# Optimization experiments

Hardware: AMD Instinct MI355X
Metric: run time of the kernel (lower is better)

The kernel has to match this reference:

```python
import jax, jax.numpy as jnp
import numpy as np

N_NODES = 100000
N_EDGES = 1600000
D_IN, D_H, D_OUT = 512, 128, 64
BN_EPS = 1e-5


def setup_inputs() -> dict:
    key = jax.random.key(0)
    ks = jax.random.split(key, 8)
    x = jax.random.normal(ks[0], (N_NODES, D_IN), dtype=jnp.float32)
    # COO sparse normalized adjacency
    row = jnp.sort(jax.random.randint(ks[1], (N_EDGES,), 0, N_NODES))
    col = jax.random.randint(ks[2], (N_EDGES,), 0, N_NODES)
    adj_vals = jax.random.uniform(ks[3], (N_EDGES,), dtype=jnp.float32) / 16.0
    # GraphConvolution params (xavier_uniform weight, zero bias)
    lim0 = float(np.sqrt(6.0 / (D_IN + D_H)))
    lim1 = float(np.sqrt(6.0 / (D_H + D_OUT)))
    W0 = jax.random.uniform(ks[4], (D_IN, D_H), minval=-lim0, maxval=lim0, dtype=jnp.float32)
    W1 = jax.random.uniform(ks[5], (D_H, D_OUT), minval=-lim1, maxval=lim1, dtype=jnp.float32)
    b0 = jnp.zeros((D_H,), dtype=jnp.float32)
    b1 = jnp.zeros((D_OUT,), dtype=jnp.float32)
    return {"x": x, "W0": W0, "b0": b0, "W1": W1, "b1": b1,
            "adj_vals": adj_vals, "row": row, "col": col}


def _spmm(vals, row, col, h, n):
    # (sparse adj) @ h : gather source rows, scale by edge value, scatter-add to dest
    return jax.ops.segment_sum(vals[:, None] * h[col], row, num_segments=n)


def reference(x, W0, b0, W1, b1, adj_vals, row, col):
    n = x.shape[0]
    # layer 0: adj @ (x @ W0) + b0  (dropout is identity in eval mode)
    h = _spmm(adj_vals, row, col, x @ W0, n) + b0
    h = jax.nn.relu(h)
    # BatchNorm1d(affine=False, track_running_stats=False): batch stats, biased var
    mean = jnp.mean(h, axis=0)
    var = jnp.mean(jnp.square(h - mean), axis=0)
    h = (h - mean) * jax.lax.rsqrt(var + BN_EPS)
    # layer 1: adj @ (h @ W1) + b1
    return _spmm(adj_vals, row, col, h @ W1, n) + b1
```

## Files before the change

kernel.cpp:

```cpp
#include <hip/hip_runtime.h>
#include <hip/hip_bf16.h>
#include <cstdint>
#include <cstddef>

#define D_IN  512
#define D_H   128
#define D_OUT 64
#define SB    512

typedef __attribute__((ext_vector_type(8))) short bf16x8;
typedef __attribute__((ext_vector_type(4))) float f32x4;

__device__ __forceinline__ float bf2f(unsigned short u) {
  union { unsigned int i; float f; } v; v.i = ((unsigned int)u) << 16; return v.f;
}
__device__ __forceinline__ unsigned short f2bf(float f) {
  union { unsigned int i; float f; } v; v.f = f;
  unsigned int r = v.i + 0x7FFFu + ((v.i >> 16) & 1u);
  return (unsigned short)(r >> 16);
}
__device__ __forceinline__ unsigned int pk_bf16(float a, float b) {
  union { __hip_bfloat162 h; unsigned int u; } cv;
  cv.h = __float22bfloat162_rn(make_float2(a, b));
  return cv.u;
}

#define OFF_RP    0u
#define OFF_W0T   400384u
#define OFF_W1TP  531456u
#define OFF_CVEC  547840u
#define OFF_PSUM  548096u
#define OFF_PSQ   810240u
#define OFF_H     1072384u
#define END_H     26672384u
#define END_HW    39472384u

__global__ void k_init(const int* __restrict__ row, int* __restrict__ rp,
                       const float* __restrict__ W0, unsigned short* __restrict__ W0t,
                       int n, int e, int RB) {
  int b = blockIdx.x, t = threadIdx.x;
  if (b < RB) {
    int i = b * 256 + t;
    if (i > n) return;
    int lo = 0, hi = e;
    while (lo < hi) { int mid = (lo + hi) >> 1; if (row[mid] < i) lo = mid + 1; else hi = mid; }
    rp[i] = lo;
  } else {
    int idx = (b - RB) * 256 + t;
    int k = idx & (D_IN - 1);
    int nn = idx >> 9;
    W0t[nn * D_IN + k] = f2bf(W0[k * D_H + nn]);
  }
}

__global__ __launch_bounds__(256) void k_gemm1(const float* __restrict__ A,
                                               const unsigned short* __restrict__ Bt,
                                               unsigned short* __restrict__ C,
                                               int M) {
  __shared__ unsigned short Ash[2][4 * 128 * 8];
  __shared__ unsigned short Bsh[2][4 * 128 * 8];
  const int tid  = threadIdx.x;
  const int lane = tid & 63;
  const int wave = tid >> 6;
  const int wm = (wave >> 1) * 64;
  const int wn = (wave & 1) * 64;
  const int m0 = blockIdx.x * 128;
  const int quad = lane >> 4;
  const int l16  = lane & 15;
  f32x4 acc[4][4] = {};

  int am[2], ak[2];
  const float* aptr[2];
  const unsigned short* bptr[2];
#pragma unroll
  for (int i = 0; i < 2; ++i) {
    int c = tid + i * 256;
    am[i] = c >> 2; ak[i] = c & 3;
    int gm = m0 + am[i]; if (gm >= M) gm = M - 1;
    aptr[i] = A  + (size_t)gm * D_IN + ak[i] * 8;
    bptr[i] = Bt + (size_t)am[i] * D_IN + ak[i] * 8;
  }

  f32x4 areg[2][2];
  bf16x8 breg[2];
#pragma unroll
  for (int i = 0; i < 2; ++i) {
    areg[i][0] = *(const f32x4*)(aptr[i]);
    areg[i][1] = *(const f32x4*)(aptr[i] + 4);
    breg[i]    = *(const bf16x8*)(bptr[i]);
  }

  const int NIT = D_IN / 32;
  for (int it = 0; it < NIT; ++it) {
    const int buf = it & 1;
    unsigned short* ash = Ash[buf];
    unsigned short* bsh = Bsh[buf];
#pragma unroll
    for (int i = 0; i < 2; ++i) {
      unsigned int pk4[4];
      pk4[0] = pk_bf16(areg[i][0][0], areg[i][0][1]);
      pk4[1] = pk_bf16(areg[i][0][2], areg[i][0][3]);
      pk4[2] = pk_bf16(areg[i][1][0], areg[i][1][1]);
      pk4[3] = pk_bf16(areg[i][1][2], areg[i][1][3]);
      *(uint4*)&ash[(ak[i] * 128 + am[i]) * 8] = *(uint4*)pk4;
      *(bf16x8*)&bsh[(ak[i] * 128 + am[i]) * 8] = breg[i];
    }
    __syncthreads();
    if (it + 1 < NIT) {
      int k0 = (it + 1) * 32;
#pragma unroll
      for (int i = 0; i < 2; ++i) {
        areg[i][0] = *(const f32x4*)(aptr[i] + k0);
        areg[i][1] = *(const f32x4*)(aptr[i] + k0 + 4);
        breg[i]    = *(const bf16x8*)(bptr[i] + k0);
      }
    }
    bf16x8 af[4], bfv[4];
#pragma unroll
    for (int mf = 0; mf < 4; ++mf)
      af[mf] = *(const bf16x8*)&ash[(quad * 128 + (wm + mf * 16 + l16)) * 8];
#pragma unroll
    for (int nf = 0; nf < 4; ++nf)
      bfv[nf] = *(const bf16x8*)&bsh[(quad * 128 + (wn + nf * 16 + l16)) * 8];
#pragma unroll
    for (int mf = 0; mf < 4; ++mf)
#pragma unroll
      for (int nf = 0; nf < 4; ++nf)
        acc[mf][nf] = __builtin_amdgcn_mfma_f32_16x16x32_bf16(af[mf], bfv[nf], acc[mf][nf], 0, 0, 0);
  }
#pragma unroll
  for (int mf = 0; mf < 4; ++mf)
#pragma unroll
    for (int nf = 0; nf < 4; ++nf)
#pragma unroll
      for (int i = 0; i < 4; ++i) {
        int r = m0 + wm + mf * 16 + quad * 4 + i;
        int cc = wn + nf * 16 + l16;
        if (r < M) C[(size_t)r * D_H + cc] = f2bf(acc[mf][nf][i]);
      }
}

__global__ __launch_bounds__(256) void k_spmm1(const unsigned int* __restrict__ xw2,
                                               const float* __restrict__ adj,
                                               const int* __restrict__ col,
                                               const int* __restrict__ rp,
                                               const float* __restrict__ b0,
                                               unsigned int* __restrict__ h2,
                                               int n) {
  int node = blockIdx.x * 4 + (threadIdx.x >> 6);
  if (node >= n) return;
  int l = threadIdx.x & 63;
  int e0 = rp[node], e1 = rp[node + 1];
  float a0 = 0.f, a1 = 0.f;
  for (int e = e0; e < e1; e += 16) {
    int idx[16]; float w[16];
#pragma unroll
    for (int j = 0; j < 16; ++j) {
      int ee = e + j;
      int ec = ee < e1 ? ee : e0;
      idx[j] = col[ec];
      w[j] = ee < e1 ? adj[ec] : 0.f;
    }
#pragma unroll
    for (int j = 0; j < 16; ++j) {
      unsigned int p = xw2[(size_t)idx[j] * 64 + l];
      a0 += w[j] * bf2f((unsigned short)(p & 0xFFFF));
      a1 += w[j] * bf2f((unsigned short)(p >> 16));
    }
  }
  float r0 = fmaxf(a0 + b0[2 * l], 0.f);
  float r1 = fmaxf(a1 + b0[2 * l + 1], 0.f);
  h2[(size_t)node * 64 + l] = ((unsigned int)f2bf(r1) << 16) | (unsigned int)f2bf(r0);
}

__global__ __launch_bounds__(256) void k_stats(const unsigned int* __restrict__ h2,
                                               float* __restrict__ psum,
                                               float* __restrict__ psq, int n) {
  __shared__ float sA[256], sB[256], qA[256], qB[256];
  int t = threadIdx.x;
  int f2 = t & 63, rg = t >> 6;
  float s0 = 0.f, s1 = 0.f, q0 = 0.f, q1 = 0.f;
  for (int r = blockIdx.x * 4 + rg; r < n; r += gridDim.x * 4) {
    unsigned int p = h2[(size_t)r * 64 + f2];
    float v0 = bf2f((unsigned short)(p & 0xFFFF));
    float v1 = bf2f((unsigned short)(p >> 16));
    s0 += v0; s1 += v1; q0 += v0 * v0; q1 += v1 * v1;
  }
  sA[t] = s0; sB[t] = s1; qA[t] = q0; qB[t] = q1;
  __syncthreads();
  if (t < 64) {
    float S0 = sA[t] + sA[t + 64] + sA[t + 128] + sA[t + 192];
    float S1 = sB[t] + sB[t + 64] + sB[t + 128] + sB[t + 192];
    float Q0 = qA[t] + qA[t + 64] + qA[t + 128] + qA[t + 192];
    float Q1 = qB[t] + qB[t + 64] + qB[t + 128] + qB[t + 192];
    psum[blockIdx.x * 128 + 2 * t]     = S0;
    psum[blockIdx.x * 128 + 2 * t + 1] = S1;
    psq [blockIdx.x * 128 + 2 * t]     = Q0;
    psq [blockIdx.x * 128 + 2 * t + 1] = Q1;
  }
}

__global__ void k_prep2(const float* __restrict__ psum, const float* __restrict__ psq,
                        const float* __restrict__ W1,
                        unsigned short* __restrict__ W1tp, float* __restrict__ cvec,
                        int n) {
  __shared__ float mean_s[128], istd_s[128];
  int t = threadIdx.x;
  if (t < 128) {
    float s = 0.f, q = 0.f;
#pragma unroll 4
    for (int b = 0; b < SB; ++b) { s += psum[b * 128 + t]; q += psq[b * 128 + t]; }
    float m = s / (float)n;
    float var = q / (float)n - m * m;
    if (var < 0.f) var = 0.f;
    mean_s[t] = m;
    istd_s[t] = rsqrtf(var + 1e-5f);
  }
  __syncthreads();
  for (int idx = t; idx < D_OUT * D_H; idx += 256) {
    int nn = idx >> 7, k = idx & 127;
    W1tp[nn * D_H + k] = f2bf(istd_s[k] * W1[k * D_OUT + nn]);
  }
  if (t < D_OUT) {
    float a = 0.f;
    for (int k = 0; k < D_H; ++k) a += mean_s[k] * istd_s[k] * W1[k * D_OUT + t];
    cvec[t] = -a;
  }
}

__global__ __launch_bounds__(256) void k_gemm2(const unsigned short* __restrict__ A,
                                               const unsigned short* __restrict__ Bt,
                                               const float* __restrict__ cvec,
                                               unsigned short* __restrict__ Cout,
                                               int M) {
  __shared__ unsigned short Ash[4 * 128 * 8];
  __shared__ unsigned short Bsh[4 * 64 * 8];
  const int tid  = threadIdx.x;
  const int lane = tid & 63;
  const int wave = tid >> 6;
  const int wm = wave * 32;
  const int m0 = blockIdx.x * 128;
  const int quad = lane >> 4;
  const int l16  = lane & 15;
  f32x4 acc[2][4] = {};

  for (int k0 = 0; k0 < D_H; k0 += 32) {
    __syncthreads();
#pragma unroll
    for (int i = 0; i < 2; ++i) {
      int c = tid + i * 256;
      int m = c >> 2, k8 = c & 3;
      int gm = m0 + m; if (gm >= M) gm = M - 1;
      *(bf16x8*)&Ash[(k8 * 128 + m) * 8] =
          *(const bf16x8*)&A[(size_t)gm * D_H + k0 + k8 * 8];
    }
    {
      int nn = tid >> 2, k8 = tid & 3;
      *(bf16x8*)&Bsh[(k8 * 64 + nn) * 8] =
          *(const bf16x8*)&Bt[(size_t)nn * D_H + k0 + k8 * 8];
    }
    __syncthreads();
    bf16x8 af[2], bfv[4];
#pragma unroll
    for (int mf = 0; mf < 2; ++mf)
      af[mf] = *(const bf16x8*)&Ash[(quad * 128 + (wm + mf * 16 + l16)) * 8];
#pragma unroll
    for (int nf = 0; nf < 4; ++nf)
      bfv[nf] = *(const bf16x8*)&Bsh[(quad * 64 + (nf * 16 + l16)) * 8];
#pragma unroll
    for (int mf = 0; mf < 2; ++mf)
#pragma unroll
      for (int nf = 0; nf < 4; ++nf)
        acc[mf][nf] = __builtin_amdgcn_mfma_f32_16x16x32_bf16(af[mf], bfv[nf], acc[mf][nf], 0, 0, 0);
  }
#pragma unroll
  for (int mf = 0; mf < 2; ++mf)
#pragma unroll
    for (int nf = 0; nf < 4; ++nf)
#pragma unroll
      for (int i = 0; i < 4; ++i) {
        int r = m0 + wm + mf * 16 + quad * 4 + i;
        int cc = nf * 16 + l16;
        if (r < M) Cout[(size_t)r * 64 + cc] = f2bf(acc[mf][nf][i] + cvec[cc]);
      }
}

__global__ __launch_bounds__(256) void k_spmm2(const unsigned int* __restrict__ hw2,
                                               const float* __restrict__ adj,
                                               const int* __restrict__ col,
                                               const int* __restrict__ rp,
                                               const float* __restrict__ b1,
                                               float2* __restrict__ o2,
                                               int n) {
  int node = blockIdx.x * 8 + (threadIdx.x >> 5);
  if (node >= n) return;
  int l = threadIdx.x & 31;
  int e0 = rp[node], e1 = rp[node + 1];
  float a0 = 0.f, a1 = 0.f;
  for (int e = e0; e < e1; e += 16) {
    int idx[16]; float w[16];
#pragma unroll
    for (int j = 0; j < 16; ++j) {
      int ee = e + j;
      int ec = ee < e1 ? ee : e0;
      idx[j] = col[ec];
      w[j] = ee < e1 ? adj[ec] : 0.f;
    }
#pragma unroll
    for (int j = 0; j < 16; ++j) {
      unsigned int p = hw2[(size_t)idx[j] * 32 + l];
      a0 += w[j] * bf2f((unsigned short)(p & 0xFFFF));
      a1 += w[j] * bf2f((unsigned short)(p >> 16));
    }
  }
  float2 r; r.x = a0 + b1[2 * l]; r.y = a1 + b1[2 * l + 1];
  o2[(size_t)node * 32 + l] = r;
}

extern "C" void kernel_launch(void* const* d_in, const int* in_sizes, int n_in,
                              void* d_out, int out_size, void* d_ws, size_t ws_size,
                              hipStream_t stream) {
  const float* x   = (const float*)d_in[0];
  const float* W0  = (const float*)d_in[1];
  const float* b0  = (const float*)d_in[2];
  const float* W1  = (const float*)d_in[3];
  const float* b1  = (const float*)d_in[4];
  const float* adj = (const float*)d_in[5];
  const int* row = (const int*)d_in[6];
  const int* col = (const int*)d_in[7];
  const int N = in_sizes[0] / D_IN;
  const int E = in_sizes[5];

  char* ws = (char*)d_ws;
  int*            rp   = (int*)(ws + OFF_RP);
  unsigned short* W0t  = (unsigned short*)(ws + OFF_W0T);
  unsigned short* W1tp = (unsigned short*)(ws + OFF_W1TP);
  float*          cvec = (float*)(ws + OFF_CVEC);
  float*          psum = (float*)(ws + OFF_PSUM);
  float*          psq  = (float*)(ws + OFF_PSQ);
  unsigned short* h    = (unsigned short*)(ws + OFF_H);

  unsigned short* xw = (unsigned short*)d_out;
  const bool hw_in_ws = (ws_size >= (size_t)END_HW);
  unsigned short* hw   = hw_in_ws ? (unsigned short*)(ws + END_H) : (unsigned short*)d_out;
  float*          outd = hw_in_ws ? (float*)d_out                 : (float*)(ws + OFF_H);

  const int RB = (N + 1 + 255) / 256;
  const int TB = (D_IN * D_H) / 256;
  k_init<<<RB + TB, 256, 0, stream>>>(row, rp, W0, W0t, N, E, RB);

  k_gemm1<<<(N + 127) / 128, 256, 0, stream>>>(x, W0t, xw, N);
  k_spmm1<<<(N + 3) / 4, 256, 0, stream>>>((const unsigned int*)xw, adj, col, rp, b0,
                                           (unsigned int*)h, N);
  k_stats<<<SB, 256, 0, stream>>>((const unsigned int*)h, psum, psq, N);
  k_prep2<<<1, 256, 0, stream>>>(psum, psq, W1, W1tp, cvec, N);
  k_gemm2<<<(N + 127) / 128, 256, 0, stream>>>(h, W1tp, cvec, hw, N);
  k_spmm2<<<(N + 7) / 8, 256, 0, stream>>>((const unsigned int*)hw, adj, col, rp, b1,
                                           (float2*)outd, N);

  if (!hw_in_ws) {
    hipMemcpyAsync(d_out, outd, (size_t)N * D_OUT * sizeof(float),
                   hipMemcpyDeviceToDevice, stream);
  }
}
```

Before: 515.5 us.

## Fuse GCN pipeline into one cooperative persistent kernel with grid syncs

Replaces the seven-kernel launch sequence with a single cooperative kernel of 512 persistent blocks. Each phase (row pointers, GEMM1, SpMM1 with fused BN statistics, BN prep, GEMM2, SpMM2) loops over tiles and is separated by grid-wide syncs. This removes per-kernel launch overhead and the separate stats pass over h, since stats are accumulated during SpMM1. The cost is a fixed grid size that may limit occupancy and latency hiding in the gather-heavy SpMM phases, plus grid.sync overhead, with the old path kept as a fallback.

```diff
diff --git a/kernel.cpp b/kernel.cpp
--- a/kernel.cpp
+++ b/kernel.cpp
@@ -1,11 +1,15 @@
 #include <hip/hip_runtime.h>
+#include <hip/hip_cooperative_groups.h>
 #include <hip/hip_bf16.h>
 #include <cstdint>
 #include <cstddef>
 
+namespace cg = cooperative_groups;
+
 #define D_IN  512
 #define D_H   128
 #define D_OUT 64
+#define GRID  512
 #define SB    512
 
 typedef __attribute__((ext_vector_type(8))) short bf16x8;
@@ -34,6 +38,275 @@
 #define OFF_H     1072384u
 #define END_H     26672384u
 #define END_HW    39472384u
+
+__global__ __launch_bounds__(256, 2) void gcn_mega(
+    const float* __restrict__ x, const float* __restrict__ W0,
+    const float* __restrict__ b0, const float* __restrict__ W1,
+    const float* __restrict__ b1, const float* __restrict__ adj,
+    const int* __restrict__ row, const int* __restrict__ col,
+    char* __restrict__ ws, unsigned short* __restrict__ xw16,
+    float2* __restrict__ outv, int N, int E) {
+  __shared__ union {
+    struct { unsigned short A[2][4096]; unsigned short B[2][4096]; } g1;
+    struct { float sA[256], sB[256], qA[256], qB[256]; } st;
+    struct { unsigned short A[4096]; unsigned short B[2048]; } g2;
+    struct { float mean[128]; float istd[128]; } pp;
+  } sh;
+
+  cg::grid_group grid = cg::this_grid();
+  const int G   = gridDim.x;
+  const int bid = blockIdx.x;
+  const int tid = threadIdx.x;
+  const int lane = tid & 63;
+  const int wave = tid >> 6;
+  const int quad = lane >> 4;
+  const int l16  = lane & 15;
+
+  int*            rp   = (int*)(ws + OFF_RP);
+  unsigned short* W0t  = (unsigned short*)(ws + OFF_W0T);
+  unsigned short* W1tp = (unsigned short*)(ws + OFF_W1TP);
+  float*          cvec = (float*)(ws + OFF_CVEC);
+  float*          psum = (float*)(ws + OFF_PSUM);
+  float*          psq  = (float*)(ws + OFF_PSQ);
+  unsigned short* h    = (unsigned short*)(ws + OFF_H);
+  unsigned int*   h2   = (unsigned int*)h;
+  unsigned short* hw   = (unsigned short*)(ws + END_H);
+  unsigned int*   hw2  = (unsigned int*)hw;
+  unsigned int*   xw2  = (unsigned int*)xw16;
+
+  for (int i = bid * 256 + tid; i <= N; i += G * 256) {
+    int lo = 0, hi = E;
+    while (lo < hi) { int mid = (lo + hi) >> 1; if (row[mid] < i) lo = mid + 1; else hi = mid; }
+    rp[i] = lo;
+  }
+  for (int idx = bid * 256 + tid; idx < D_IN * D_H; idx += G * 256) {
+    int k = idx & (D_IN - 1);
+    int nn = idx >> 9;
+    W0t[nn * D_IN + k] = f2bf(W0[k * D_H + nn]);
+  }
+  __threadfence(); grid.sync();
+
+  const int T1 = (N + 127) / 128;
+  for (int t = bid; t < T1; t += G) {
+    const int m0 = t * 128;
+    const int wm = (wave >> 1) * 64;
+    const int wn = (wave & 1) * 64;
+    f32x4 acc[4][4] = {};
+    int am[2], ak[2];
+    const float* aptr[2];
+    const unsigned short* bptr[2];
+#pragma unroll
+    for (int i = 0; i < 2; ++i) {
+      int c = tid + i * 256;
+      am[i] = c >> 2; ak[i] = c & 3;
+      int gm = m0 + am[i]; if (gm >= N) gm = N - 1;
+      aptr[i] = x   + (size_t)gm * D_IN + ak[i] * 8;
+      bptr[i] = W0t + (size_t)am[i] * D_IN + ak[i] * 8;
+    }
+    f32x4 areg[2][2];
+    bf16x8 breg[2];
+#pragma unroll
+    for (int i = 0; i < 2; ++i) {
+      areg[i][0] = *(const f32x4*)(aptr[i]);
+      areg[i][1] = *(const f32x4*)(aptr[i] + 4);
+      breg[i]    = *(const bf16x8*)(bptr[i]);
+    }
+    const int NIT = D_IN / 32;
+    for (int it = 0; it < NIT; ++it) {
+      const int buf = it & 1;
+      unsigned short* ash = sh.g1.A[buf];
+      unsigned short* bsh = sh.g1.B[buf];
+#pragma unroll
+      for (int i = 0; i < 2; ++i) {
+        unsigned int pk4[4];
+        pk4[0] = pk_bf16(areg[i][0][0], areg[i][0][1]);
+        pk4[1] = pk_bf16(areg[i][0][2], areg[i][0][3]);
+        pk4[2] = pk_bf16(areg[i][1][0], areg[i][1][1]);
+        pk4[3] = pk_bf16(areg[i][1][2], areg[i][1][3]);
+        *(uint4*)&ash[(ak[i] * 128 + am[i]) * 8] = *(uint4*)pk4;
+        *(bf16x8*)&bsh[(ak[i] * 128 + am[i]) * 8] = breg[i];
+      }
+      __syncthreads();
+      if (it + 1 < NIT) {
+        int k0 = (it + 1) * 32;
+#pragma unroll
+        for (int i = 0; i < 2; ++i) {
+          areg[i][0] = *(const f32x4*)(aptr[i] + k0);
+          areg[i][1] = *(const f32x4*)(aptr[i] + k0 + 4);
+          breg[i]    = *(const bf16x8*)(bptr[i] + k0);
+        }
+      }
+      bf16x8 af[4], bfv[4];
+#pragma unroll
+      for (int mf = 0; mf < 4; ++mf)
+        af[mf] = *(const bf16x8*)&ash[(quad * 128 + (wm + mf * 16 + l16)) * 8];
+#pragma unroll
+      for (int nf = 0; nf < 4; ++nf)
+        bfv[nf] = *(const bf16x8*)&bsh[(quad * 128 + (wn + nf * 16 + l16)) * 8];
+#pragma unroll
+      for (int mf = 0; mf < 4; ++mf)
+#pragma unroll
+        for (int nf = 0; nf < 4; ++nf)
+          acc[mf][nf] = __builtin_amdgcn_mfma_f32_16x16x32_bf16(af[mf], bfv[nf], acc[mf][nf], 0, 0, 0);
+    }
+#pragma unroll
+    for (int mf = 0; mf < 4; ++mf)
+#pragma unroll
+      for (int nf = 0; nf < 4; ++nf)
+#pragma unroll
+        for (int i = 0; i < 4; ++i) {
+          int r = m0 + wm + mf * 16 + quad * 4 + i;
+          int cc = wn + nf * 16 + l16;
+          if (r < N) xw16[(size_t)r * D_H + cc] = f2bf(acc[mf][nf][i]);
+        }
+    __syncthreads();
+  }
+  __threadfence(); grid.sync();
+
+  {
+    float s0 = 0.f, s1 = 0.f, q0 = 0.f, q1 = 0.f;
+    const int VB = (N + 3) / 4;
+    for (int vb = bid; vb < VB; vb += G) {
+      int node = vb * 4 + wave;
+      if (node >= N) continue;
+      int e0 = rp[node], e1 = rp[node + 1];
+      float a0 = 0.f, a1 = 0.f;
+      for (int e = e0; e < e1; e += 16) {
+        int idx[16]; float w[16];
+#pragma unroll
+        for (int j = 0; j < 16; ++j) {
+          int ee = e + j;
+          int ec = ee < e1 ? ee : e0;
+          idx[j] = col[ec];
+          w[j] = ee < e1 ? adj[ec] : 0.f;
+        }
+#pragma unroll
+        for (int j = 0; j < 16; ++j) {
+          unsigned int p = xw2[(size_t)idx[j] * 64 + lane];
+          a0 += w[j] * bf2f((unsigned short)(p & 0xFFFF));
+          a1 += w[j] * bf2f((unsigned short)(p >> 16));
+        }
+      }
+      float r0 = fmaxf(a0 + b0[2 * lane], 0.f);
+      float r1 = fmaxf(a1 + b0[2 * lane + 1], 0.f);
+      h2[(size_t)node * 64 + lane] = ((unsigned int)f2bf(r1) << 16) | (unsigned int)f2bf(r0);
+      s0 += r0; s1 += r1; q0 += r0 * r0; q1 += r1 * r1;
+    }
+    sh.st.sA[tid] = s0; sh.st.sB[tid] = s1; sh.st.qA[tid] = q0; sh.st.qB[tid] = q1;
+    __syncthreads();
+    if (tid < 64) {
+      float S0 = sh.st.sA[tid] + sh.st.sA[tid + 64] + sh.st.sA[tid + 128] + sh.st.sA[tid + 192];
+      float S1 = sh.st.sB[tid] + sh.st.sB[tid + 64] + sh.st.sB[tid + 128] + sh.st.sB[tid + 192];
+      float Q0 = sh.st.qA[tid] + sh.st.qA[tid + 64] + sh.st.qA[tid + 128] + sh.st.qA[tid + 192];
+      float Q1 = sh.st.qB[tid] + sh.st.qB[tid + 64] + sh.st.qB[tid + 128] + sh.st.qB[tid + 192];
+      psum[bid * 128 + 2 * tid]     = S0;
+      psum[bid * 128 + 2 * tid + 1] = S1;
+      psq [bid * 128 + 2 * tid]     = Q0;
+      psq [bid * 128 + 2 * tid + 1] = Q1;
+    }
+  }
+  __threadfence(); grid.sync();
+
+  if (bid == 0) {
+    if (tid < 128) {
+      float s = 0.f, q = 0.f;
+      for (int b = 0; b < G; ++b) { s += psum[b * 128 + tid]; q += psq[b * 128 + tid]; }
+      float m = s / (float)N;
+      float var = q / (float)N - m * m;
+      if (var < 0.f) var = 0.f;
+      sh.pp.mean[tid] = m;
+      sh.pp.istd[tid] = rsqrtf(var + 1e-5f);
+    }
+    __syncthreads();
+    for (int idx = tid; idx < D_OUT * D_H; idx += 256) {
+      int nn = idx >> 7, k = idx & 127;
+      W1tp[nn * D_H + k] = f2bf(sh.pp.istd[k] * W1[k * D_OUT + nn]);
+    }
+    if (tid < D_OUT) {
+      float a = 0.f;
+      for (int k = 0; k < D_H; ++k) a += sh.pp.mean[k] * sh.pp.istd[k] * W1[k * D_OUT + tid];
+      cvec[tid] = -a;
+    }
+  }
+  __threadfence(); grid.sync();
+
+  for (int t = bid; t < T1; t += G) {
+    const int m0 = t * 128;
+    const int wm = wave * 32;
+    f32x4 acc[2][4] = {};
+    for (int k0 = 0; k0 < D_H; k0 += 32) {
+      __syncthreads();
+#pragma unroll
+      for (int i = 0; i < 2; ++i) {
+        int c = tid + i * 256;
+        int m = c >> 2, k8 = c & 3;
+        int gm = m0 + m; if (gm >= N) gm = N - 1;
+        *(bf16x8*)&sh.g2.A[(k8 * 128 + m) * 8] =
+            *(const bf16x8*)&h[(size_t)gm * D_H + k0 + k8 * 8];
+      }
+      {
+        int nn = tid >> 2, k8 = tid & 3;
+        *(bf16x8*)&sh.g2.B[(k8 * 64 + nn) * 8] =
+            *(const bf16x8*)&W1tp[(size_t)nn * D_H + k0 + k8 * 8];
+      }
+      __syncthreads();
+      bf16x8 af[2], bfv[4];
+#pragma unroll
+      for (int mf = 0; mf < 2; ++mf)
+        af[mf] = *(const bf16x8*)&sh.g2.A[(quad * 128 + (wm + mf * 16 + l16)) * 8];
+#pragma unroll
+      for (int nf = 0; nf < 4; ++nf)
+        bfv[nf] = *(const bf16x8*)&sh.g2.B[(quad * 64 + (nf * 16 + l16)) * 8];
+#pragma unroll
+      for (int mf = 0; mf < 2; ++mf)
+#pragma unroll
+        for (int nf = 0; nf < 4; ++nf)
+          acc[mf][nf] = __builtin_amdgcn_mfma_f32_16x16x32_bf16(af[mf], bfv[nf], acc[mf][nf], 0, 0, 0);
+    }
+#pragma unroll
+    for (int mf = 0; mf < 2; ++mf)
+#pragma unroll
+      for (int nf = 0; nf < 4; ++nf)
+#pragma unroll
+        for (int i = 0; i < 4; ++i) {
+          int r = m0 + wm + mf * 16 + quad * 4 + i;
+          int cc = nf * 16 + l16;
+          if (r < N) hw[(size_t)r * 64 + cc] = f2bf(acc[mf][nf][i] + cvec[cc]);
+        }
+    __syncthreads();
+  }
+  __threadfence(); grid.sync();
+
+  {
+    const int VB = (N + 7) / 8;
+    const int hwv = tid >> 5;
+    const int l   = tid & 31;
+    for (int vb = bid; vb < VB; vb += G) {
+      int node = vb * 8 + hwv;
+      if (node >= N) continue;
+      int e0 = rp[node], e1 = rp[node + 1];
+      float a0 = 0.f, a1 = 0.f;
+      for (int e = e0; e < e1; e += 16) {
+        int idx[16]; float w[16];
+#pragma unroll
+        for (int j = 0; j < 16; ++j) {
+          int ee = e + j;
+          int ec = ee < e1 ? ee : e0;
+          idx[j] = col[ec];
+          w[j] = ee < e1 ? adj[ec] : 0.f;
+        }
+#pragma unroll
+        for (int j = 0; j < 16; ++j) {
+          unsigned int p = hw2[(size_t)idx[j] * 32 + l];
+          a0 += w[j] * bf2f((unsigned short)(p & 0xFFFF));
+          a1 += w[j] * bf2f((unsigned short)(p >> 16));
+        }
+      }
+      float2 r; r.x = a0 + b1[2 * l]; r.y = a1 + b1[2 * l + 1];
+      outv[(size_t)node * 32 + l] = r;
+    }
+  }
+}
 
 __global__ void k_init(const int* __restrict__ row, int* __restrict__ rp,
                        const float* __restrict__ W0, unsigned short* __restrict__ W0t,
@@ -55,20 +328,13 @@
 
 __global__ __launch_bounds__(256) void k_gemm1(const float* __restrict__ A,
                                                const unsigned short* __restrict__ Bt,
-                                               unsigned short* __restrict__ C,
-                                               int M) {
-  __shared__ unsigned short Ash[2][4 * 128 * 8];
-  __shared__ unsigned short Bsh[2][4 * 128 * 8];
-  const int tid  = threadIdx.x;
-  const int lane = tid & 63;
-  const int wave = tid >> 6;
-  const int wm = (wave >> 1) * 64;
-  const int wn = (wave & 1) * 64;
-  const int m0 = blockIdx.x * 128;
-  const int quad = lane >> 4;
-  const int l16  = lane & 15;
+                                               unsigned short* __restrict__ C, int M) {
+  __shared__ unsigned short Ash[2][4096];
+  __shared__ unsigned short Bsh[2][4096];
+  const int tid = threadIdx.x, lane = tid & 63, wave = tid >> 6;
+  const int wm = (wave >> 1) * 64, wn = (wave & 1) * 64;
+  const int m0 = blockIdx.x * 128, quad = lane >> 4, l16 = lane & 15;
   f32x4 acc[4][4] = {};
-
   int am[2], ak[2];
   const float* aptr[2];
   const unsigned short* bptr[2];
@@ -77,19 +343,16 @@
     int c = tid + i * 256;
     am[i] = c >> 2; ak[i] = c & 3;
     int gm = m0 + am[i]; if (gm >= M) gm = M - 1;
-    aptr[i] = A  + (size_t)gm * D_IN + ak[i] * 8;
+    aptr[i] = A + (size_t)gm * D_IN + ak[i] * 8;
     bptr[i] = Bt + (size_t)am[i] * D_IN + ak[i] * 8;
   }
-
-  f32x4 areg[2][2];
-  bf16x8 breg[2];
+  f32x4 areg[2][2]; bf16x8 breg[2];
 #pragma unroll
   for (int i = 0; i < 2; ++i) {
     areg[i][0] = *(const f32x4*)(aptr[i]);
     areg[i][1] = *(const f32x4*)(aptr[i] + 4);
     breg[i]    = *(const bf16x8*)(bptr[i]);
   }
-
   const int NIT = D_IN / 32;
   for (int it = 0; it < NIT; ++it) {
     const int buf = it & 1;
@@ -145,8 +408,7 @@
                                                const int* __restrict__ col,
                                                const int* __restrict__ rp,
                                                const float* __restrict__ b0,
-                                               unsigned int* __restrict__ h2,
-                                               int n) {
+                                               unsigned int* __restrict__ h2, int n) {
   int node = blockIdx.x * 4 + (threadIdx.x >> 6);
   if (node >= n) return;
   int l = threadIdx.x & 63;
@@ -202,8 +464,7 @@
 
 __global__ void k_prep2(const float* __restrict__ psum, const float* __restrict__ psq,
                         const float* __restrict__ W1,
-                        unsigned short* __restrict__ W1tp, float* __restrict__ cvec,
-                        int n) {
+                        unsigned short* __restrict__ W1tp, float* __restrict__ cvec, int n) {
   __shared__ float mean_s[128], istd_s[128];
   int t = threadIdx.x;
   if (t < 128) {
@@ -231,19 +492,13 @@
 __global__ __launch_bounds__(256) void k_gemm2(const unsigned short* __restrict__ A,
                                                const unsigned short* __restrict__ Bt,
                                                const float* __restrict__ cvec,
-                                               unsigned short* __restrict__ Cout,
-                                               int M) {
-  __shared__ unsigned short Ash[4 * 128 * 8];
-  __shared__ unsigned short Bsh[4 * 64 * 8];
-  const int tid  = threadIdx.x;
-  const int lane = tid & 63;
-  const int wave = tid >> 6;
-  const int wm = wave * 32;
-  const int m0 = blockIdx.x * 128;
-  const int quad = lane >> 4;
-  const int l16  = lane & 15;
+                                               unsigned short* __restrict__ Cout, int M) {
+  __shared__ unsigned short Ash[4096];
+  __shared__ unsigned short Bsh[2048];
+  const int tid = threadIdx.x, lane = tid & 63, wave = tid >> 6;
+  const int wm = wave * 32, m0 = blockIdx.x * 128;
+  const int quad = lane >> 4, l16 = lane & 15;
   f32x4 acc[2][4] = {};
-
   for (int k0 = 0; k0 < D_H; k0 += 32) {
     __syncthreads();
 #pragma unroll
@@ -251,13 +506,11 @@
       int c = tid + i * 256;
       int m = c >> 2, k8 = c & 3;
       int gm = m0 + m; if (gm >= M) gm = M - 1;
-      *(bf16x8*)&Ash[(k8 * 128 + m) * 8] =
-          *(const bf16x8*)&A[(size_t)gm * D_H + k0 + k8 * 8];
+      *(bf16x8*)&Ash[(k8 * 128 + m) * 8] = *(const bf16x8*)&A[(size_t)gm * D_H + k0 + k8 * 8];
     }
     {
       int nn = tid >> 2, k8 = tid & 3;
-      *(bf16x8*)&Bsh[(k8 * 64 + nn) * 8] =
-          *(const bf16x8*)&Bt[(size_t)nn * D_H + k0 + k8 * 8];
+      *(bf16x8*)&Bsh[(k8 * 64 + nn) * 8] = *(const bf16x8*)&Bt[(size_t)nn * D_H + k0 + k8 * 8];
     }
     __syncthreads();
     bf16x8 af[2], bfv[4];
@@ -290,8 +543,7 @@
                                                const int* __restrict__ col,
                                                const int* __restrict__ rp,
                                                const float* __restrict__ b1,
-                                               float2* __restrict__ o2,
-                                               int n) {
+                                               float2* __restrict__ o2, int n) {
   int node = blockIdx.x * 8 + (threadIdx.x >> 5);
   if (node >= n) return;
   int l = threadIdx.x & 31;
@@ -328,10 +580,23 @@
   const float* adj = (const float*)d_in[5];
   const int* row = (const int*)d_in[6];
   const int* col = (const int*)d_in[7];
-  const int N = in_sizes[0] / D_IN;
-  const int E = in_sizes[5];
+  int N = in_sizes[0] / D_IN;
+  int E = in_sizes[5];
 
   char* ws = (char*)d_ws;
+  unsigned short* xw16 = (unsigned short*)d_out;
+  float2*         outv = (float2*)d_out;
+
+  if (ws_size >= (size_t)END_HW) {
+    void* args[] = {(void*)&x, (void*)&W0, (void*)&b0, (void*)&W1, (void*)&b1,
+                    (void*)&adj, (void*)&row, (void*)&col, (void*)&ws,
+                    (void*)&xw16, (void*)&outv, (void*)&N, (void*)&E};
+    hipError_t err = hipLaunchCooperativeKernel((void*)gcn_mega, dim3(GRID), dim3(256),
+                                                args, 0, stream);
+    if (err == hipSuccess) return;
+    (void)hipGetLastError();
+  }
+
   int*            rp   = (int*)(ws + OFF_RP);
   unsigned short* W0t  = (unsigned short*)(ws + OFF_W0T);
   unsigned short* W1tp = (unsigned short*)(ws + OFF_W1TP);
@@ -340,24 +605,21 @@
   float*          psq  = (float*)(ws + OFF_PSQ);
   unsigned short* h    = (unsigned short*)(ws + OFF_H);
 
-  unsigned short* xw = (unsigned short*)d_out;
   const bool hw_in_ws = (ws_size >= (size_t)END_HW);
-  unsigned short* hw   = hw_in_ws ? (unsigned short*)(ws + END_H) : (unsigned short*)d_out;
+  unsigned short* hwp  = hw_in_ws ? (unsigned short*)(ws + END_H) : (unsigned short*)d_out;
   float*          outd = hw_in_ws ? (float*)d_out                 : (float*)(ws + OFF_H);
 
   const int RB = (N + 1 + 255) / 256;
   const int TB = (D_IN * D_H) / 256;
   k_init<<<RB + TB, 256, 0, stream>>>(row, rp, W0, W0t, N, E, RB);
-
-  k_gemm1<<<(N + 127) / 128, 256, 0, stream>>>(x, W0t, xw, N);
-  k_spmm1<<<(N + 3) / 4, 256, 0, stream>>>((const unsigned int*)xw, adj, col, rp, b0,
+  k_gemm1<<<(N + 127) / 128, 256, 0, stream>>>(x, W0t, xw16, N);
+  k_spmm1<<<(N + 3) / 4, 256, 0, stream>>>((const unsigned int*)xw16, adj, col, rp, b0,
                                            (unsigned int*)h, N);
   k_stats<<<SB, 256, 0, stream>>>((const unsigned int*)h, psum, psq, N);
   k_prep2<<<1, 256, 0, stream>>>(psum, psq, W1, W1tp, cvec, N);
-  k_gemm2<<<(N + 127) / 128, 256, 0, stream>>>(h, W1tp, cvec, hw, N);
-  k_spmm2<<<(N + 7) / 8, 256, 0, stream>>>((const unsigned int*)hw, adj, col, rp, b1,
+  k_gemm2<<<(N + 127) / 128, 256, 0, stream>>>(h, W1tp, cvec, hwp, N);
+  k_spmm2<<<(N + 7) / 8, 256, 0, stream>>>((const unsigned int*)hwp, adj, col, rp, b1,
                                            (float2*)outd, N);
-
   if (!hw_in_ws) {
     hipMemcpyAsync(d_out, outd, (size_t)N * D_OUT * sizeof(float),
                    hipMemcpyDeviceToDevice, stream);
```

Result: slower. 1.239 ms (+140.4%).
